# Optimization experiments

Measured on AMD Instinct MI355X. Metric: run time of the kernel, lower is better.

Reference implementation:

```python
import jax, jax.numpy as jnp
import numpy as np

B, T, D, H = 256, 200, 128, 128


def setup_inputs() -> dict:
    key = jax.random.key(0)
    ks = jax.random.split(key, 6)
    return {
        "x": jax.random.normal(ks[0], (B, T, D), dtype=jnp.float32),
        "duration": jax.random.uniform(ks[1], (B, T), dtype=jnp.float32),
        "rep_indicies": jax.random.randint(ks[2], (B,), 0, T),
        "W_x": jax.random.normal(ks[3], (D, 7 * H), dtype=jnp.float32) / np.float32(np.sqrt(D)),
        "W_h": jax.random.normal(ks[4], (H, 7 * H), dtype=jnp.float32) / np.float32(np.sqrt(H)),
        "b": jnp.zeros((7 * H,), dtype=jnp.float32),
    }


def _ctlstm(x, duration, W_x, W_h, b):
    # Neural-Hawkes continuous-time LSTM scan. x:[B,T,D], duration:[B,T]
    xg = jnp.einsum("btd,dg->btg", x, W_x) + b  # [B,T,7H] precomputed input gates

    def step(carry, inputs):
        h, c_t, cbar = carry  # each [B,H]
        xg_t, dt = inputs     # [B,7H], [B]
        g = xg_t + h @ W_h
        i, f, z, o, ibar, fbar, d = jnp.split(g, 7, axis=-1)
        i, f, o = jax.nn.sigmoid(i), jax.nn.sigmoid(f), jax.nn.sigmoid(o)
        ibar, fbar = jax.nn.sigmoid(ibar), jax.nn.sigmoid(fbar)
        z = jnp.tanh(z)
        delta = jax.nn.softplus(d)
        c = f * c_t + i * z               # cell right after the event
        cbar_new = fbar * cbar + ibar * z  # target cell it decays toward
        c_new = cbar_new + (c - cbar_new) * jnp.exp(-delta * dt[:, None])
        h_new = o * jnp.tanh(c_new)
        return (h_new, c_new, cbar_new), (h_new, c_new)

    z0 = jnp.zeros((x.shape[0], W_h.shape[0]), dtype=x.dtype)
    _, (h_seq, c_seq) = jax.lax.scan(
        step, (z0, z0, z0), (jnp.swapaxes(xg, 0, 1), jnp.swapaxes(duration, 0, 1))
    )
    # h_seq/c_seq: [T,B,H] -> [B,T,H]
    return jnp.swapaxes(h_seq, 0, 1), jnp.swapaxes(c_seq, 0, 1)


def _gather_state(s, rep_indicies):
    # s:[B,T,H]; pick per-sample time index -> [1,B,H]
    idx = jnp.broadcast_to(rep_indicies[:, None, None], (s.shape[0], 1, s.shape[2]))
    return jnp.take_along_axis(s, idx, axis=1)[:, 0, :][None]


def reference(x, duration, rep_indicies, W_x, W_h, b):
    # Dropout is identity in eval mode.
    h_seq, c_seq = _ctlstm(x, duration, W_x, W_h, b)
    return (_gather_state(h_seq, rep_indicies), _gather_state(c_seq, rep_indicies))
```

## Files before the change

### kernel.cpp

```cpp
#include <hip/hip_runtime.h>

#define TT 200
#define BB 256
#define DD 128
#define HH 128
#define NG 896
#define NGP 1024

typedef _Float16 half8 __attribute__((ext_vector_type(8)));
typedef _Float16 half4 __attribute__((ext_vector_type(4)));
typedef float float4v __attribute__((ext_vector_type(4)));
typedef int int4v __attribute__((ext_vector_type(4)));

__device__ __forceinline__ float rcpf_(float x) { return __builtin_amdgcn_rcpf(x); }
__device__ __forceinline__ float sigmoidf_(float x) { return rcpf_(1.f + __expf(-x)); }
__device__ __forceinline__ float tanhf_(float x) { return 1.f - 2.f * rcpf_(__expf(2.f * x) + 1.f); }
__device__ __forceinline__ float softplusf_(float x) {
  return fmaxf(x, 0.f) + 0.69314718056f * __log2f(1.f + __expf(-fabsf(x)));
}

__global__ __launch_bounds__(256) void wtrans_k(const float* __restrict__ Wx,
    const float* __restrict__ bias, _Float16* __restrict__ WxTp, float* __restrict__ bias_p) {
  int idx = blockIdx.x * 256 + threadIdx.x;
  if (idx < NGP * DD) {
    int pcol = idx >> 7, k = idx & 127;
    int u = pcol >> 3, g = pcol & 7;
    WxTp[idx] = (g < 7) ? (_Float16)Wx[k * NG + g * HH + u] : (_Float16)0.f;
  } else if (idx < NGP * DD + NGP) {
    int pcol = idx - NGP * DD;
    int u = pcol >> 3, g = pcol & 7;
    bias_p[pcol] = (g < 7) ? bias[g * HH + u] : 0.f;
  }
}

__global__ __launch_bounds__(256) void wquant_k(const float* __restrict__ Wh,
    char* __restrict__ WhQ, float* __restrict__ wscale) {
  __shared__ float redmax[4][64];
  int tid = threadIdx.x;
  int c = tid & 63, kq = tid >> 6;
  int col = blockIdx.x * 64 + c;
  float v[32];
  float m = 0.f;
#pragma unroll
  for (int i = 0; i < 32; ++i) {
    v[i] = Wh[(size_t)(kq * 32 + i) * NG + col];
    m = fmaxf(m, fabsf(v[i]));
  }
  redmax[kq][c] = m;
  __syncthreads();
  float mm = fmaxf(fmaxf(redmax[0][c], redmax[1][c]),
                   fmaxf(redmax[2][c], redmax[3][c]));
  mm = mm > 0.f ? mm : 1.f;
  float inv = 127.f * rcpf_(mm);
  char q[32];
#pragma unroll
  for (int i = 0; i < 32; ++i) q[i] = (char)__float2int_rn(v[i] * inv);
#pragma unroll
  for (int i = 0; i < 8; ++i)
    *(int*)&WhQ[(size_t)col * DD + kq * 32 + i * 4] = *(int*)&q[i * 4];
  if (kq == 0) wscale[col] = mm * (1.f / 127.f);
}

__global__ __launch_bounds__(256, 2) void xg_gemm_k(const float* __restrict__ x,
    const _Float16* __restrict__ WxTp, const float* __restrict__ bias_p,
    _Float16* __restrict__ xg, int t0) {
  int mt = blockIdx.x;
  __shared__ _Float16 Ald[128][136];
  __shared__ _Float16 Bld[128][136];
  int tid = threadIdx.x;
  int G0 = mt * 128;
  int t = t0 + (G0 >> 8);
  int b0 = G0 & 255;
  {
    int r = tid >> 5, kq = (tid & 31) << 2;
#pragma unroll
    for (int it = 0; it < 16; ++it) {
      int row = r + it * 8;
      float4v xv = *(const float4v*)(x + ((size_t)(b0 + row) * TT + t) * DD + kq);
      half4 h4 = {(_Float16)xv[0], (_Float16)xv[1], (_Float16)xv[2], (_Float16)xv[3]};
      *(half4*)&Ald[row][kq] = h4;
    }
  }
  __syncthreads();
  int wv = tid >> 6, l = tid & 63, lr = l & 15, lk8 = (l >> 4) << 3;
  half8 af[2][4];
#pragma unroll
  for (int mf = 0; mf < 2; ++mf)
#pragma unroll
    for (int kk = 0; kk < 4; ++kk)
      af[mf][kk] = *(const half8*)&Ald[wv * 32 + mf * 16 + lr][kk * 32 + lk8];
  int r4 = (l >> 4) << 2;

  for (int nt = 0; nt < 8; ++nt) {
    for (int i = tid; i < 128 * 16; i += 256) {
      int r = i >> 4, c8 = (i & 15) << 3;
      *(half8*)&Bld[r][c8] = *(const half8*)(WxTp + (size_t)(nt * 128 + r) * DD + c8);
    }
    __syncthreads();
    float4v acc[2][8];
#pragma unroll
    for (int a = 0; a < 2; ++a)
#pragma unroll
      for (int q = 0; q < 8; ++q) acc[a][q] = (float4v){0.f, 0.f, 0.f, 0.f};
#pragma unroll
    for (int kk = 0; kk < 4; ++kk) {
#pragma unroll
      for (int nf = 0; nf < 8; ++nf) {
        half8 bv = *(const half8*)&Bld[nf * 16 + lr][kk * 32 + lk8];
        acc[0][nf] = __builtin_amdgcn_mfma_f32_16x16x32_f16(af[0][kk], bv, acc[0][nf], 0, 0, 0);
        acc[1][nf] = __builtin_amdgcn_mfma_f32_16x16x32_f16(af[1][kk], bv, acc[1][nf], 0, 0, 0);
      }
    }
#pragma unroll
    for (int nf = 0; nf < 8; ++nf) {
      int colL = nf * 16 + lr;
      float bv = bias_p[nt * 128 + colL];
#pragma unroll
      for (int mf = 0; mf < 2; ++mf) {
        int rowL = wv * 32 + mf * 16 + r4;
#pragma unroll
        for (int rr = 0; rr < 4; ++rr)
          Ald[rowL + rr][colL] = (_Float16)(acc[mf][nf][rr] + bv);
      }
    }
    __syncthreads();
#pragma unroll
    for (int it = 0; it < 8; ++it) {
      int slot = tid + it * 256;
      int row = slot >> 4, cg = slot & 15;
      half8 v = *(const half8*)&Ald[row][cg * 8];
      *(half8*)&xg[(size_t)(G0 + row) * NGP + nt * 128 + cg * 8] = v;
    }
  }
}

__global__ __launch_bounds__(512, 2) void rec_k(const _Float16* __restrict__ xg,
    const float* __restrict__ dur, const int* __restrict__ rep,
    const char* __restrict__ WhQ, const float* __restrict__ wscale,
    float* __restrict__ out,
    char* __restrict__ st_h, float* __restrict__ st_c, float* __restrict__ st_cb,
    int t0, int t1) {
  int b = blockIdx.x, j = threadIdx.x;
  int tend = rep[b];
  if (t0 > tend) return;
  int tstop = min(t1 - 1, tend);
  __shared__ __align__(16) char hq[2][HH];
  __shared__ float dlds[TT];
  int w = j >> 6, l = j & 63, lr = l & 15, lg = l >> 4;
  int u = w * 16 + lr;

  int4v wbq[7][2];
#pragma unroll
  for (int g = 0; g < 7; ++g)
#pragma unroll
    for (int m = 0; m < 2; ++m)
      wbq[g][m] = *(const int4v*)(WhQ + (size_t)(g * HH + u) * DD + m * 64 + lg * 16);
  float sg[7];
#pragma unroll
  for (int g = 0; g < 7; ++g) sg[g] = wscale[g * HH + u] * (1.f / 127.f);
  for (int i = j; i < TT; i += 512) dlds[i] = dur[b * TT + i];
  float c_s = 0.f, cb_s = 0.f;
  if (lg == 0) {
    hq[0][u] = (t0 == 0) ? (char)0 : st_h[b * HH + u];
    hq[1][u] = (char)0;
  }
  if (t0 != 0) {
    c_s = st_c[b * HH + u];
    cb_s = st_cb[b * HH + u];
  }
  __syncthreads();

  const _Float16* xgp = xg + (size_t)b * NGP + u * 8;
  const size_t stp = (size_t)BB * NGP;
  half8 cur[8], nxt[8];
#pragma unroll
  for (int i = 0; i < 8; ++i)
    cur[i] = *(const half8*)(xgp + (size_t)(min(t0 + i, tstop) - t0) * stp);
  char hqsave = 0;

#define STEP(T, CUR, PIN, POUT)                                                  \
  do {                                                                           \
    float dt = dlds[T];                                                          \
    int4v aq0 = *(const int4v*)&hq[PIN][lg * 16];                                \
    int4v aq1 = *(const int4v*)&hq[PIN][64 + lg * 16];                           \
    int4v acc[7];                                                                \
    _Pragma("unroll") for (int g = 0; g < 7; ++g) acc[g] = (int4v){0, 0, 0, 0};  \
    _Pragma("unroll") for (int g = 0; g < 7; ++g)                                \
        acc[g] = __builtin_amdgcn_mfma_i32_16x16x64_i8(aq0, wbq[g][0], acc[g], 0, 0, 0); \
    _Pragma("unroll") for (int g = 0; g < 7; ++g)                                \
        acc[g] = __builtin_amdgcn_mfma_i32_16x16x64_i8(aq1, wbq[g][1], acc[g], 0, 0, 0); \
    float gv[7];                                                                 \
    _Pragma("unroll") for (int g = 0; g < 7; ++g)                                \
        gv[g] = (float)acc[g][0] * sg[g] + (float)CUR[g];                        \
    float iv = sigmoidf_(gv[0]), fv = sigmoidf_(gv[1]);                          \
    float zv = tanhf_(gv[2]), ov = sigmoidf_(gv[3]);                             \
    float ibv = sigmoidf_(gv[4]), fbv = sigmoidf_(gv[5]);                        \
    float dv = softplusf_(gv[6]);                                                \
    float cc = fv * c_s + iv * zv;                                               \
    cb_s = fbv * cb_s + ibv * zv;                                                \
    float cn = cb_s + (cc - cb_s) * __expf(-dv * dt);                            \
    float hn = ov * tanhf_(cn);                                                  \
    c_s = cn;                                                                    \
    char hb = (char)__float2int_rn(hn * 127.f);                                  \
    hqsave = hb;                                                                 \
    if (lg == 0) {                                                               \
      if ((T) == tend) {                                                         \
        out[b * HH + u] = hn;                                                    \
        out[BB * HH + b * HH + u] = cn;                                          \
      }                                                                          \
      hq[POUT][u] = hb;                                                          \
    }                                                                            \
    __syncthreads();                                                             \
  } while (0)

  for (int tb = t0; tb <= tstop; tb += 8) {
#pragma unroll
    for (int i = 0; i < 8; ++i)
      nxt[i] = *(const half8*)(xgp + (size_t)(min(tb + 8 + i, tstop) - t0) * stp);
    STEP(tb, cur[0], 0, 1);
    if (tb + 1 <= tstop) STEP(tb + 1, cur[1], 1, 0);
    if (tb + 2 <= tstop) STEP(tb + 2, cur[2], 0, 1);
    if (tb + 3 <= tstop) STEP(tb + 3, cur[3], 1, 0);
    if (tb + 4 <= tstop) STEP(tb + 4, cur[4], 0, 1);
    if (tb + 5 <= tstop) STEP(tb + 5, cur[5], 1, 0);
    if (tb + 6 <= tstop) STEP(tb + 6, cur[6], 0, 1);
    if (tb + 7 <= tstop) STEP(tb + 7, cur[7], 1, 0);
#pragma unroll
    for (int i = 0; i < 8; ++i) cur[i] = nxt[i];
  }
#undef STEP

  if (tstop < tend && lg == 0) {
    st_h[b * HH + u] = hqsave;
    st_c[b * HH + u] = c_s;
    st_cb[b * HH + u] = cb_s;
  }
}

extern "C" void kernel_launch(void* const* d_in, const int* in_sizes, int n_in,
                              void* d_out, int out_size, void* d_ws, size_t ws_size,
                              hipStream_t stream) {
  const float* x = (const float*)d_in[0];
  const float* dur = (const float*)d_in[1];
  const int* rep = (const int*)d_in[2];
  const float* Wx = (const float*)d_in[3];
  const float* Wh = (const float*)d_in[4];
  const float* bias = (const float*)d_in[5];
  float* out = (float*)d_out;
  char* ws = (char*)d_ws;

  size_t off = 0;
  _Float16* WxTp = (_Float16*)(ws + off); off += (size_t)NGP * DD * 2;
  float* bias_p = (float*)(ws + off); off += (size_t)NGP * 4;
  char* WhQ = (char*)(ws + off); off += (size_t)NG * DD;
  float* wscale = (float*)(ws + off); off += (size_t)NG * 4;
  char* st_h = (char*)(ws + off); off += (size_t)BB * HH;
  float* st_c = (float*)(ws + off); off += (size_t)BB * HH * 4;
  float* st_cb = (float*)(ws + off); off += (size_t)BB * HH * 4;
  off = (off + 255) & ~(size_t)255;
  _Float16* xgbuf = (_Float16*)(ws + off);

  size_t avail = ws_size > off ? ws_size - off : 0;
  size_t perT = (size_t)BB * NGP * 2;
  int Tc = (int)(avail / perT);
  if (Tc > TT) Tc = TT;
  if (Tc < 1) Tc = 1;

  int nprep = NGP * DD + NGP;
  hipLaunchKernelGGL(wtrans_k, dim3((nprep + 255) / 256), dim3(256), 0, stream,
                     Wx, bias, WxTp, bias_p);
  hipLaunchKernelGGL(wquant_k, dim3(NG / 64), dim3(256), 0, stream,
                     Wh, WhQ, wscale);
  for (int t0 = 0; t0 < TT; t0 += Tc) {
    int t1 = t0 + Tc;
    if (t1 > TT) t1 = TT;
    int mtiles = (t1 - t0) * BB / 128;
    hipLaunchKernelGGL(xg_gemm_k, dim3(mtiles), dim3(256), 0, stream,
                       x, WxTp, bias_p, xgbuf, t0);
    hipLaunchKernelGGL(rec_k, dim3(BB), dim3(512), 0, stream,
                       xgbuf, dur, rep, WhQ, wscale, out, st_h, st_c, st_cb, t0, t1);
  }
}
```

Before: 158.1 us.

## Pair two batch rows per recurrence block and skip dead xg stores

The recurrence kernel now handles two batch samples per 1024-thread block. Each block runs until the later of the two samples' rep index, and the two samples keep separate shared hidden-state and duration buffers. The 8-step register prefetch of xg is replaced by a per-step load, and the gate MFMAs are split into groups of 4 and 3 to reduce register pressure. The xg GEMM no longer writes timesteps past each sample's rep index, and the two weight-prep kernels are merged into one launch. Risks: the exposed per-step global load latency, the tight register budget implied by launch_bounds(1024,4), and the shorter sample in each pair doing wasted work on unwritten xg values.

```diff
diff --git a/kernel.cpp b/kernel.cpp
--- a/kernel.cpp
+++ b/kernel.cpp
@@ -19,26 +19,30 @@
   return fmaxf(x, 0.f) + 0.69314718056f * __log2f(1.f + __expf(-fabsf(x)));
 }
 
-__global__ __launch_bounds__(256) void wtrans_k(const float* __restrict__ Wx,
-    const float* __restrict__ bias, _Float16* __restrict__ WxTp, float* __restrict__ bias_p) {
-  int idx = blockIdx.x * 256 + threadIdx.x;
-  if (idx < NGP * DD) {
-    int pcol = idx >> 7, k = idx & 127;
-    int u = pcol >> 3, g = pcol & 7;
-    WxTp[idx] = (g < 7) ? (_Float16)Wx[k * NG + g * HH + u] : (_Float16)0.f;
-  } else if (idx < NGP * DD + NGP) {
-    int pcol = idx - NGP * DD;
-    int u = pcol >> 3, g = pcol & 7;
-    bias_p[pcol] = (g < 7) ? bias[g * HH + u] : 0.f;
-  }
-}
-
-__global__ __launch_bounds__(256) void wquant_k(const float* __restrict__ Wh,
+#define WT_BLKS 516
+
+__global__ __launch_bounds__(256) void prep_k(const float* __restrict__ Wx,
+    const float* __restrict__ bias, const float* __restrict__ Wh,
+    _Float16* __restrict__ WxTp, float* __restrict__ bias_p,
     char* __restrict__ WhQ, float* __restrict__ wscale) {
+  int bx = blockIdx.x;
+  if (bx < WT_BLKS) {
+    int idx = bx * 256 + threadIdx.x;
+    if (idx < NGP * DD) {
+      int pcol = idx >> 7, k = idx & 127;
+      int u = pcol >> 3, g = pcol & 7;
+      WxTp[idx] = (g < 7) ? (_Float16)Wx[k * NG + g * HH + u] : (_Float16)0.f;
+    } else if (idx < NGP * DD + NGP) {
+      int pcol = idx - NGP * DD;
+      int u = pcol >> 3, g = pcol & 7;
+      bias_p[pcol] = (g < 7) ? bias[g * HH + u] : 0.f;
+    }
+    return;
+  }
   __shared__ float redmax[4][64];
   int tid = threadIdx.x;
   int c = tid & 63, kq = tid >> 6;
-  int col = blockIdx.x * 64 + c;
+  int col = (bx - WT_BLKS) * 64 + c;
   float v[32];
   float m = 0.f;
 #pragma unroll
@@ -63,14 +67,16 @@
 
 __global__ __launch_bounds__(256, 2) void xg_gemm_k(const float* __restrict__ x,
     const _Float16* __restrict__ WxTp, const float* __restrict__ bias_p,
-    _Float16* __restrict__ xg, int t0) {
+    const int* __restrict__ rep, _Float16* __restrict__ xg, int t0) {
   int mt = blockIdx.x;
   __shared__ _Float16 Ald[128][136];
   __shared__ _Float16 Bld[128][136];
+  __shared__ int tends[128];
   int tid = threadIdx.x;
   int G0 = mt * 128;
   int t = t0 + (G0 >> 8);
   int b0 = G0 & 255;
+  if (tid < 128) tends[tid] = rep[b0 + tid];
   {
     int r = tid >> 5, kq = (tid & 31) << 2;
 #pragma unroll
@@ -128,24 +134,30 @@
     for (int it = 0; it < 8; ++it) {
       int slot = tid + it * 256;
       int row = slot >> 4, cg = slot & 15;
-      half8 v = *(const half8*)&Ald[row][cg * 8];
-      *(half8*)&xg[(size_t)(G0 + row) * NGP + nt * 128 + cg * 8] = v;
-    }
-  }
-}
-
-__global__ __launch_bounds__(512, 2) void rec_k(const _Float16* __restrict__ xg,
+      if (t <= tends[row]) {
+        half8 v = *(const half8*)&Ald[row][cg * 8];
+        *(half8*)&xg[(size_t)(G0 + row) * NGP + nt * 128 + cg * 8] = v;
+      }
+    }
+  }
+}
+
+__global__ __launch_bounds__(1024, 4) void rec_k(const _Float16* __restrict__ xg,
     const float* __restrict__ dur, const int* __restrict__ rep,
     const char* __restrict__ WhQ, const float* __restrict__ wscale,
     float* __restrict__ out,
     char* __restrict__ st_h, float* __restrict__ st_c, float* __restrict__ st_cb,
     int t0, int t1) {
-  int b = blockIdx.x, j = threadIdx.x;
-  int tend = rep[b];
-  if (t0 > tend) return;
-  int tstop = min(t1 - 1, tend);
-  __shared__ __align__(16) char hq[2][HH];
-  __shared__ float dlds[TT];
+  int tid = threadIdx.x;
+  int s = tid >> 9, j = tid & 511;
+  int b0 = blockIdx.x * 2, b = b0 + s;
+  int tendA = rep[b0], tendB = rep[b0 + 1];
+  int tmax = max(tendA, tendB);
+  if (t0 > tmax) return;
+  int tend = s ? tendB : tendA;
+  int tstop = min(t1 - 1, tmax);
+  __shared__ __align__(16) char hq[2][2][HH];
+  __shared__ float dlds[2][TT];
   int w = j >> 6, l = j & 63, lr = l & 15, lg = l >> 4;
   int u = w * 16 + lr;
 
@@ -158,11 +170,14 @@
   float sg[7];
 #pragma unroll
   for (int g = 0; g < 7; ++g) sg[g] = wscale[g * HH + u] * (1.f / 127.f);
-  for (int i = j; i < TT; i += 512) dlds[i] = dur[b * TT + i];
+  for (int i = tid; i < 2 * TT; i += 1024) {
+    int ss = i / TT, ii = i - ss * TT;
+    dlds[ss][ii] = dur[(b0 + ss) * TT + ii];
+  }
   float c_s = 0.f, cb_s = 0.f;
   if (lg == 0) {
-    hq[0][u] = (t0 == 0) ? (char)0 : st_h[b * HH + u];
-    hq[1][u] = (char)0;
+    hq[0][s][u] = (t0 == 0) ? (char)0 : st_h[b * HH + u];
+    hq[1][s][u] = (char)0;
   }
   if (t0 != 0) {
     c_s = st_c[b * HH + u];
@@ -172,26 +187,35 @@
 
   const _Float16* xgp = xg + (size_t)b * NGP + u * 8;
   const size_t stp = (size_t)BB * NGP;
-  half8 cur[8], nxt[8];
-#pragma unroll
-  for (int i = 0; i < 8; ++i)
-    cur[i] = *(const half8*)(xgp + (size_t)(min(t0 + i, tstop) - t0) * stp);
   char hqsave = 0;
 
-#define STEP(T, CUR, PIN, POUT)                                                  \
+#define STEP(T, PIN, POUT)                                                       \
   do {                                                                           \
-    float dt = dlds[T];                                                          \
-    int4v aq0 = *(const int4v*)&hq[PIN][lg * 16];                                \
-    int4v aq1 = *(const int4v*)&hq[PIN][64 + lg * 16];                           \
-    int4v acc[7];                                                                \
-    _Pragma("unroll") for (int g = 0; g < 7; ++g) acc[g] = (int4v){0, 0, 0, 0};  \
-    _Pragma("unroll") for (int g = 0; g < 7; ++g)                                \
+    half8 xv = *(const half8*)(xgp + (size_t)((T) - t0) * stp);                  \
+    float dt = dlds[s][T];                                                       \
+    int4v aq0 = *(const int4v*)&hq[PIN][s][lg * 16];                             \
+    int4v aq1 = *(const int4v*)&hq[PIN][s][64 + lg * 16];                        \
+    float gv[7];                                                                 \
+    {                                                                            \
+      int4v acc[4];                                                              \
+      _Pragma("unroll") for (int g = 0; g < 4; ++g) {                            \
+        acc[g] = (int4v){0, 0, 0, 0};                                            \
         acc[g] = __builtin_amdgcn_mfma_i32_16x16x64_i8(aq0, wbq[g][0], acc[g], 0, 0, 0); \
-    _Pragma("unroll") for (int g = 0; g < 7; ++g)                                \
         acc[g] = __builtin_amdgcn_mfma_i32_16x16x64_i8(aq1, wbq[g][1], acc[g], 0, 0, 0); \
-    float gv[7];                                                                 \
-    _Pragma("unroll") for (int g = 0; g < 7; ++g)                                \
-        gv[g] = (float)acc[g][0] * sg[g] + (float)CUR[g];                        \
+      }                                                                          \
+      _Pragma("unroll") for (int g = 0; g < 4; ++g)                              \
+          gv[g] = (float)acc[g][0] * sg[g] + (float)xv[g];                       \
+    }                                                                            \
+    {                                                                            \
+      int4v acc[3];                                                              \
+      _Pragma("unroll") for (int g = 0; g < 3; ++g) {                            \
+        acc[g] = (int4v){0, 0, 0, 0};                                            \
+        acc[g] = __builtin_amdgcn_mfma_i32_16x16x64_i8(aq0, wbq[g + 4][0], acc[g], 0, 0, 0); \
+        acc[g] = __builtin_amdgcn_mfma_i32_16x16x64_i8(aq1, wbq[g + 4][1], acc[g], 0, 0, 0); \
+      }                                                                          \
+      _Pragma("unroll") for (int g = 0; g < 3; ++g)                              \
+          gv[g + 4] = (float)acc[g][0] * sg[g + 4] + (float)xv[g + 4];           \
+    }                                                                            \
     float iv = sigmoidf_(gv[0]), fv = sigmoidf_(gv[1]);                          \
     float zv = tanhf_(gv[2]), ov = sigmoidf_(gv[3]);                             \
     float ibv = sigmoidf_(gv[4]), fbv = sigmoidf_(gv[5]);                        \
@@ -208,25 +232,14 @@
         out[b * HH + u] = hn;                                                    \
         out[BB * HH + b * HH + u] = cn;                                          \
       }                                                                          \
-      hq[POUT][u] = hb;                                                          \
+      hq[POUT][s][u] = hb;                                                       \
     }                                                                            \
     __syncthreads();                                                             \
   } while (0)
 
-  for (int tb = t0; tb <= tstop; tb += 8) {
-#pragma unroll
-    for (int i = 0; i < 8; ++i)
-      nxt[i] = *(const half8*)(xgp + (size_t)(min(tb + 8 + i, tstop) - t0) * stp);
-    STEP(tb, cur[0], 0, 1);
-    if (tb + 1 <= tstop) STEP(tb + 1, cur[1], 1, 0);
-    if (tb + 2 <= tstop) STEP(tb + 2, cur[2], 0, 1);
-    if (tb + 3 <= tstop) STEP(tb + 3, cur[3], 1, 0);
-    if (tb + 4 <= tstop) STEP(tb + 4, cur[4], 0, 1);
-    if (tb + 5 <= tstop) STEP(tb + 5, cur[5], 1, 0);
-    if (tb + 6 <= tstop) STEP(tb + 6, cur[6], 0, 1);
-    if (tb + 7 <= tstop) STEP(tb + 7, cur[7], 1, 0);
-#pragma unroll
-    for (int i = 0; i < 8; ++i) cur[i] = nxt[i];
+  for (int t = t0; t <= tstop; t += 2) {
+    STEP(t, 0, 1);
+    if (t + 1 <= tstop) STEP(t + 1, 1, 0);
   }
 #undef STEP
 
@@ -266,18 +279,15 @@
   if (Tc > TT) Tc = TT;
   if (Tc < 1) Tc = 1;
 
-  int nprep = NGP * DD + NGP;
-  hipLaunchKernelGGL(wtrans_k, dim3((nprep + 255) / 256), dim3(256), 0, stream,
-                     Wx, bias, WxTp, bias_p);
-  hipLaunchKernelGGL(wquant_k, dim3(NG / 64), dim3(256), 0, stream,
-                     Wh, WhQ, wscale);
+  hipLaunchKernelGGL(prep_k, dim3(WT_BLKS + NG / 64), dim3(256), 0, stream,
+                     Wx, bias, Wh, WxTp, bias_p, WhQ, wscale);
   for (int t0 = 0; t0 < TT; t0 += Tc) {
     int t1 = t0 + Tc;
     if (t1 > TT) t1 = TT;
     int mtiles = (t1 - t0) * BB / 128;
     hipLaunchKernelGGL(xg_gemm_k, dim3(mtiles), dim3(256), 0, stream,
-                       x, WxTp, bias_p, xgbuf, t0);
-    hipLaunchKernelGGL(rec_k, dim3(BB), dim3(512), 0, stream,
+                       x, WxTp, bias_p, rep, xgbuf, t0);
+    hipLaunchKernelGGL(rec_k, dim3(BB / 2), dim3(1024), 0, stream,
                        xgbuf, dur, rep, WhQ, wscale, out, st_h, st_c, st_cb, t0, t1);
   }
 }
```

Measured after the change: 255.6 us. 1.62x slower.
